# Kernel optimization log

Measured on AMD Instinct MI355X. Metric: run time of the kernel, lower is better.

Reference implementation:

```python
import jax, jax.numpy as jnp
import numpy as np

IMSIZE = 128; R = 2; B = 2; C = 3; D = 64; Q = 128; M = 8; ITERS = 32
N = IMSIZE * IMSIZE
EPS = 1e-8


def _build_edges(S, r):
    # local (2r+1)^2 pixel neighborhood, as in build_perception(imsize, perception_size)
    ys, xs = np.meshgrid(np.arange(S), np.arange(S), indexing='ij')
    rows, cols = [], []
    for dy in range(-r, r + 1):
        for dx in range(-r, r + 1):
            ny, nx = ys + dy, xs + dx
            ok = (ny >= 0) & (ny < S) & (nx >= 0) & (nx < S)
            rows.append((ys * S + xs)[ok])
            cols.append((ny * S + nx)[ok])
    return (np.concatenate(rows).astype(np.int32), np.concatenate(cols).astype(np.int32))


def _conv(x, w, b=None):
    y = jax.lax.conv_general_dilated(x, w, (1, 1), 'SAME', dimension_numbers=('NHWC', 'HWIO', 'NHWC'))
    return y if b is None else y + b


def _bn(x, g, b):
    mu = x.mean((0, 1, 2))
    var = x.var((0, 1, 2))
    return (x - mu) * jax.lax.rsqrt(var + 1e-5) * g + b


def _resblock(f, w1, g1, t1, w2, g2, t2):
    h = jax.nn.relu(_bn(_conv(f, w1), g1, t1))
    h = _bn(_conv(h, w2), g2, t2)
    return jax.nn.relu(f + h)


def _forward(x, w_bb1, b_bb1, w_bb2, b_bb2,
             w_k1, g_k1, t_k1, w_k2, g_k2, t_k2, w_kp, b_kp,
             w_q1, g_q1, t_q1, w_q2, g_q2, t_q2, w_qp,
             h0, row, col, agent_idx):
    # conv backbone (preserves spatial resolution)
    f = jax.nn.relu(_conv(x, w_bb1, b_bb1))
    f = jax.nn.relu(_conv(f, w_bb2, b_bb2))
    # key / query heads: ResidualBlock + 1x1 conv
    ks = _conv(_resblock(f, w_k1, g_k1, t_k1, w_k2, g_k2, t_k2), w_kp, b_kp).reshape(B, N, D)
    qs = _conv(_resblock(f, w_q1, g_q1, t_q1, w_q2, g_q2, t_q2), w_qp).reshape(B, N, D)
    # edge-gather cosine similarity (torch.cosine_similarity with eps=1e-8)
    qe = qs[:, row]          # [B, E, D]
    ke = ks[:, col]          # [B, E, D]
    weights = (qe * ke).sum(-1) / (
        jnp.maximum(jnp.linalg.norm(qe, axis=-1), EPS) *
        jnp.maximum(jnp.linalg.norm(ke, axis=-1), EPS))   # [B, E]

    # 32-iteration sparse adjacency propagation: h <- normalize(A @ h)
    def step(h, _):
        msg = jnp.zeros_like(h).at[:, row, :].add(weights[:, :, None] * h[:, col, :])
        h = msg / jnp.maximum(jnp.linalg.norm(msg, axis=-1, keepdims=True), EPS)
        return h, None

    h, _ = jax.lax.scan(step, h0, None, length=ITERS)     # [B, N, Q]

    # competition routing: pixels compete for M agent slots via cosine affinity
    pix = h / jnp.maximum(jnp.linalg.norm(h, axis=-1, keepdims=True), EPS)
    ag = pix[:, agent_idx]                                # [B, M, Q]
    sim = jnp.einsum('bnq,bmq->bnm', pix, ag)
    masks = jax.nn.softmax(sim * 10.0, axis=-1)           # [B, N, M]
    return masks.reshape(B, IMSIZE, IMSIZE, M).transpose(0, 3, 1, 2)  # [B, M, W, H]


def setup_inputs() -> dict:
    key = jax.random.key(0)
    k = jax.random.split(key, 12)
    s = 0.05
    row, col = _build_edges(IMSIZE, R)
    agent_idx = np.linspace(0, N - 1, M).astype(np.int32)
    return dict(
        x=jax.random.normal(k[0], (B, IMSIZE, IMSIZE, C), jnp.float32),
        w_bb1=jax.random.normal(k[1], (3, 3, C, D), jnp.float32) * s, b_bb1=jnp.zeros((D,), jnp.float32),
        w_bb2=jax.random.normal(k[2], (3, 3, D, D), jnp.float32) * s, b_bb2=jnp.zeros((D,), jnp.float32),
        w_k1=jax.random.normal(k[3], (3, 3, D, D), jnp.float32) * s,
        g_k1=jnp.ones((D,), jnp.float32), t_k1=jnp.zeros((D,), jnp.float32),
        w_k2=jax.random.normal(k[4], (3, 3, D, D), jnp.float32) * s,
        g_k2=jnp.ones((D,), jnp.float32), t_k2=jnp.zeros((D,), jnp.float32),
        w_kp=jax.random.normal(k[5], (1, 1, D, D), jnp.float32) * s, b_kp=jnp.zeros((D,), jnp.float32),
        w_q1=jax.random.normal(k[6], (3, 3, D, D), jnp.float32) * s,
        g_q1=jnp.ones((D,), jnp.float32), t_q1=jnp.zeros((D,), jnp.float32),
        w_q2=jax.random.normal(k[7], (3, 3, D, D), jnp.float32) * s,
        g_q2=jnp.ones((D,), jnp.float32), t_q2=jnp.zeros((D,), jnp.float32),
        w_qp=jax.random.normal(k[8], (1, 1, D, D), jnp.float32) * s,
        h0=jax.random.normal(k[9], (B, N, Q), jnp.float32),
        row=jnp.asarray(row), col=jnp.asarray(col),
        agent_idx=jnp.asarray(agent_idx),
    )


def reference(x, w_bb1, b_bb1, w_bb2, b_bb2,
              w_k1, g_k1, t_k1, w_k2, g_k2, t_k2, w_kp, b_kp,
              w_q1, g_q1, t_q1, w_q2, g_q2, t_q2, w_qp,
              h0, row, col, agent_idx):
    return _forward(x, w_bb1, b_bb1, w_bb2, b_bb2,
                    w_k1, g_k1, t_k1, w_k2, g_k2, t_k2, w_kp, b_kp,
                    w_q1, g_q1, t_q1, w_q2, g_q2, t_q2, w_qp,
                    h0, row, col, agent_idx)
```

## Files before the change

### kernel.cpp

```cpp
#include <hip/hip_runtime.h>
#include <math.h>

#define NPIX 16384
#define EPSF 1e-8f

typedef float f32x4 __attribute__((ext_vector_type(4)));
typedef short s16x8 __attribute__((ext_vector_type(8)));

__device__ __forceinline__ float wred64(float s){
  s += __shfl_xor(s, 32); s += __shfl_xor(s, 16); s += __shfl_xor(s, 8);
  s += __shfl_xor(s, 4);  s += __shfl_xor(s, 2);  s += __shfl_xor(s, 1);
  return s;
}
__device__ __forceinline__ float rdlane(float v, int l){
  return __int_as_float(__builtin_amdgcn_readlane(__float_as_int(v), l));
}
__device__ __forceinline__ float dot4f(float4 a, float4 b, float acc){
  acc = fmaf(a.x,b.x,acc); acc = fmaf(a.y,b.y,acc);
  acc = fmaf(a.z,b.z,acc); acc = fmaf(a.w,b.w,acc);
  return acc;
}
__device__ __forceinline__ void bf16split(float v, unsigned short &hi, unsigned short &lo){
  unsigned u = __float_as_uint(v);
  unsigned r = u + 0x7FFFu + ((u >> 16) & 1u);
  hi = (unsigned short)(r >> 16);
  float hf = __uint_as_float(((unsigned)hi) << 16);
  float l = v - hf;
  unsigned u2 = __float_as_uint(l);
  unsigned r2 = u2 + 0x7FFFu + ((u2 >> 16) & 1u);
  lo = (unsigned short)(r2 >> 16);
}
__device__ __forceinline__ unsigned bf16rne(float x){
  unsigned u = __float_as_uint(x);
  return (u + 0x7FFFu + ((u >> 16) & 1u)) >> 16;
}

__global__ __launch_bounds__(256) void prep_kernel(const float* __restrict__ w_bb2, const float* __restrict__ w_k1,
                            const float* __restrict__ w_k2, const float* __restrict__ w_q1,
                            const float* __restrict__ w_q2, const float* __restrict__ w_kp,
                            const float* __restrict__ w_qp, unsigned short* __restrict__ wh,
                            unsigned short* __restrict__ wl, float* __restrict__ wtp,
                            float* __restrict__ stats){
  int gid = blockIdx.x*256 + threadIdx.x;
  if (gid < 184320){
    int j = gid & 7;
    int t1 = gid >> 3;
    int lane = t1 & 63;
    int t2 = t1 >> 6;
    int kb = t2 % 18;
    int t3 = t2 / 18;
    int ct = t3 & 3;
    int c  = t3 >> 2;
    const float* src = c==0? w_bb2 : c==1? w_k1 : c==2? w_k2 : c==3? w_q1 : w_q2;
    int cout = ct*16 + (lane & 15);
    int k = kb*32 + (lane>>4)*8 + j;
    float v = src[k*64 + cout];
    unsigned short h,l; bf16split(v,h,l);
    wh[gid] = h; wl[gid] = l;
  } else if (gid < 192512){
    int t = gid - 184320; int which = t >> 12; int d = t & 4095;
    const float* src = which ? w_qp : w_kp;
    int k = d & 3, cout = (d>>2) & 63, cin4 = d >> 8;
    wtp[t] = src[(cin4*4 + k)*64 + cout];
  } else if (gid < 193024){
    stats[gid - 192512] = 0.f;
  }
}

__global__ __launch_bounds__(256) void conv1_kernel(const float* __restrict__ x, const float* __restrict__ w,
                                                    const float* __restrict__ bias, float* __restrict__ out){
  int wv = blockIdx.x*4 + (threadIdx.x >> 6);
  int c  = threadIdx.x & 63;
  int p0 = wv << 3;
  int ub = __builtin_amdgcn_readfirstlane(p0);
  int b  = ub >> 14; int i0 = ub & (NPIX-1);
  int y  = i0 >> 7, x0 = i0 & 127;
  float wv_[9][3];
  #pragma unroll
  for (int t=0;t<9;++t)
    #pragma unroll
    for (int ci=0;ci<3;++ci) wv_[t][ci] = w[(t*3+ci)*64 + c];
  float bv = bias[c];
  float acc[8];
  #pragma unroll
  for (int p=0;p<8;++p) acc[p] = bv;
  for (int ky=0; ky<3; ++ky){
    int ny = y + ky - 1;
    if ((unsigned)ny >= 128u) continue;
    const float* rowp = x + ((b<<14) + ny*128)*3;
    for (int kx=0; kx<3; ++kx){
      int t = ky*3 + kx;
      #pragma unroll
      for (int p=0;p<8;++p){
        int col = x0 + p + kx - 1;
        if ((unsigned)col < 128u){
          const float* ip = rowp + col*3;
          acc[p] = fmaf(ip[0], wv_[t][0], acc[p]);
          acc[p] = fmaf(ip[1], wv_[t][1], acc[p]);
          acc[p] = fmaf(ip[2], wv_[t][2], acc[p]);
        }
      }
    }
  }
  float* op = out + (p0 << 6) + c;
  #pragma unroll
  for (int p=0;p<8;++p) op[p*64] = fmaxf(acc[p], 0.f);
}

__global__ __launch_bounds__(512) void conv3m_kernel(const float* __restrict__ in,
    const unsigned short* __restrict__ wh, const unsigned short* __restrict__ wl,
    const float* __restrict__ bias, int relu,
    const float* __restrict__ bnst, const float* __restrict__ bng, const float* __restrict__ bnb,
    float* __restrict__ out, float* __restrict__ ost){
  __shared__ char smem[50688];
  float* lout = (float*)smem;
  __shared__ float la[64], lb[64];
  __shared__ float ls1[64], ls2[64];
  int blk = blockIdx.x;
  int xh = blk & 1, y = (blk>>1) & 127, b = blk >> 8;
  int x0 = xh << 6;
  int tid = threadIdx.x;
  if (tid < 64){
    float a = 1.f, bo = 0.f;
    if (bnst){
      float mu  = bnst[tid] * (1.f/32768.f);
      float var = bnst[64+tid] * (1.f/32768.f) - mu*mu;
      a  = bng[tid] * rsqrtf(var + 1e-5f);
      bo = bnb[tid] - mu*a;
    }
    la[tid] = a; lb[tid] = bo;
    ls1[tid] = 0.f; ls2[tid] = 0.f;
  }
  __syncthreads();
  for (int s = tid; s < 3168; s += 512){
    int pr = s >> 4, cq = s & 15;
    int ky = pr / 66, px = pr - ky*66;
    int ny = y + ky - 1, gx = x0 - 1 + px;
    float v0=0.f, v1=0.f, v2=0.f, v3=0.f;
    if ((unsigned)ny < 128u && (unsigned)gx < 128u){
      const float* ip = in + (((b<<14) + ny*128 + gx)<<6) + (cq<<2);
      float4 t = *(const float4*)ip;
      int c0 = cq<<2;
      v0 = fmaxf(fmaf(t.x, la[c0],   lb[c0]),   0.f);
      v1 = fmaxf(fmaf(t.y, la[c0+1], lb[c0+1]), 0.f);
      v2 = fmaxf(fmaf(t.z, la[c0+2], lb[c0+2]), 0.f);
      v3 = fmaxf(fmaf(t.w, la[c0+3], lb[c0+3]), 0.f);
    }
    unsigned short h0,l0,h1,l1,h2,l2,h3,l3;
    bf16split(v0,h0,l0); bf16split(v1,h1,l1); bf16split(v2,h2,l2); bf16split(v3,h3,l3);
    int slot = (cq >> 1) ^ (pr & 7);
    int byte = pr*128 + (slot<<4) + ((cq & 1) << 3);
    *(uint2*)(smem + byte) = make_uint2((unsigned)h0 | ((unsigned)h1<<16),
                                        (unsigned)h2 | ((unsigned)h3<<16));
    *(uint2*)(smem + 25344 + byte) = make_uint2((unsigned)l0 | ((unsigned)l1<<16),
                                                (unsigned)l2 | ((unsigned)l3<<16));
  }
  __syncthreads();
  int lane = tid & 63, wid = tid >> 6;
  int pxsub = wid & 3, ch = wid >> 2;
  int col16 = lane & 15, kgrp = lane >> 4;
  f32x4 acc0 = {0.f,0.f,0.f,0.f}, acc1 = acc0, acl0 = acc0, acl1 = acc0;
  int abase = (ch*2*18)*512 + lane*8;
  #pragma unroll
  for (int kb=0; kb<18; ++kb){
    int tap = kb >> 1;
    int ky = (tap >= 6) ? 2 : (tap >= 3 ? 1 : 0);
    int kx = tap - ky*3;
    int pr = ky*66 + pxsub*16 + col16 + kx;
    int ci0 = ((kb & 1) << 5) + (kgrp << 3);
    int byte = pr*128 + ((((ci0 >> 3) ^ (pr & 7))) << 4);
    s16x8 Bh = *(const s16x8*)(smem + byte);
    s16x8 Bl = *(const s16x8*)(smem + 25344 + byte);
    int ao = abase + kb*512;
    s16x8 Ah0 = *(const s16x8*)(wh + ao);
    s16x8 Al0 = *(const s16x8*)(wl + ao);
    s16x8 Ah1 = *(const s16x8*)(wh + ao + 9216);
    s16x8 Al1 = *(const s16x8*)(wl + ao + 9216);
    acc0 = __builtin_amdgcn_mfma_f32_16x16x32_bf16(Ah0, Bh, acc0, 0, 0, 0);
    acl0 = __builtin_amdgcn_mfma_f32_16x16x32_bf16(Ah0, Bl, acl0, 0, 0, 0);
    acc1 = __builtin_amdgcn_mfma_f32_16x16x32_bf16(Ah1, Bh, acc1, 0, 0, 0);
    acl1 = __builtin_amdgcn_mfma_f32_16x16x32_bf16(Ah1, Bl, acl1, 0, 0, 0);
    acl0 = __builtin_amdgcn_mfma_f32_16x16x32_bf16(Al0, Bh, acl0, 0, 0, 0);
    acl1 = __builtin_amdgcn_mfma_f32_16x16x32_bf16(Al1, Bh, acl1, 0, 0, 0);
  }
  acc0 = acc0 + acl0;
  acc1 = acc1 + acl1;
  __syncthreads();
  int pxl = pxsub*16 + col16;
  int co0 = ch*32 + kgrp*4;
  *(f32x4*)(lout + pxl*68 + co0)      = acc0;
  *(f32x4*)(lout + pxl*68 + co0 + 16) = acc1;
  __syncthreads();
  {
    int px = tid >> 3, c8 = (tid & 7) << 3;
    const float* lp = lout + px*68 + c8;
    float r0[8];
    #pragma unroll
    for (int j=0;j<8;++j) r0[j] = lp[j];
    if (bias){
      #pragma unroll
      for (int j=0;j<8;++j) r0[j] += bias[c8+j];
    }
    if (relu){
      #pragma unroll
      for (int j=0;j<8;++j) r0[j] = fmaxf(r0[j], 0.f);
    }
    float* op = out + (((b<<14) + y*128 + x0 + px)<<6) + c8;
    #pragma unroll
    for (int j=0;j<8;++j) op[j] = r0[j];
    if (ost){
      float s1v[8], s2v[8];
      #pragma unroll
      for (int j=0;j<8;++j){ s1v[j] = r0[j]; s2v[j] = r0[j]*r0[j]; }
      #pragma unroll
      for (int m=8; m<64; m<<=1){
        #pragma unroll
        for (int j=0;j<8;++j){ s1v[j] += __shfl_xor(s1v[j], m); s2v[j] += __shfl_xor(s2v[j], m); }
      }
      int lane2 = tid & 63;
      if ((lane2 >> 3) == 0){
        int c0 = (lane2 & 7) << 3;
        #pragma unroll
        for (int j=0;j<8;++j){ atomicAdd(&ls1[c0+j], s1v[j]); atomicAdd(&ls2[c0+j], s2v[j]); }
      }
      __syncthreads();
      if (tid < 64){ atomicAdd(&ost[tid], ls1[tid]); atomicAdd(&ost[64+tid], ls2[tid]); }
    }
  }
}

__global__ __launch_bounds__(512) void conv3m2_kernel(const float* __restrict__ in,
    const unsigned short* __restrict__ whA, const unsigned short* __restrict__ wlA,
    const unsigned short* __restrict__ whB, const unsigned short* __restrict__ wlB,
    float* __restrict__ outA, float* __restrict__ ostA,
    float* __restrict__ outB, float* __restrict__ ostB){
  __shared__ char smem[50688];
  float* loutA = (float*)smem;
  float* loutB = (float*)smem + 4352;
  __shared__ float ls1A[64], ls2A[64], ls1B[64], ls2B[64];
  int blk = blockIdx.x;
  int xh = blk & 1, y = (blk>>1) & 127, b = blk >> 8;
  int x0 = xh << 6;
  int tid = threadIdx.x;
  if (tid < 64){ ls1A[tid]=0.f; ls2A[tid]=0.f; ls1B[tid]=0.f; ls2B[tid]=0.f; }
  __syncthreads();
  for (int s = tid; s < 3168; s += 512){
    int pr = s >> 4, cq = s & 15;
    int ky = pr / 66, px = pr - ky*66;
    int ny = y + ky - 1, gx = x0 - 1 + px;
    float v0=0.f, v1=0.f, v2=0.f, v3=0.f;
    if ((unsigned)ny < 128u && (unsigned)gx < 128u){
      const float* ip = in + (((b<<14) + ny*128 + gx)<<6) + (cq<<2);
      float4 t = *(const float4*)ip;
      v0 = t.x; v1 = t.y; v2 = t.z; v3 = t.w;
    }
    unsigned short h0,l0,h1,l1,h2,l2,h3,l3;
    bf16split(v0,h0,l0); bf16split(v1,h1,l1); bf16split(v2,h2,l2); bf16split(v3,h3,l3);
    int slot = (cq >> 1) ^ (pr & 7);
    int byte = pr*128 + (slot<<4) + ((cq & 1) << 3);
    *(uint2*)(smem + byte) = make_uint2((unsigned)h0 | ((unsigned)h1<<16),
                                        (unsigned)h2 | ((unsigned)h3<<16));
    *(uint2*)(smem + 25344 + byte) = make_uint2((unsigned)l0 | ((unsigned)l1<<16),
                                                (unsigned)l2 | ((unsigned)l3<<16));
  }
  __syncthreads();
  int lane = tid & 63, wid = tid >> 6;
  int pxsub = wid & 3, ch = wid >> 2;
  int col16 = lane & 15, kgrp = lane >> 4;
  f32x4 z = {0.f,0.f,0.f,0.f};
  f32x4 aA0=z, aA1=z, lA0=z, lA1=z, aB0=z, aB1=z, lB0=z, lB1=z;
  int abase = (ch*2*18)*512 + lane*8;
  #pragma unroll
  for (int kb=0; kb<18; ++kb){
    int tap = kb >> 1;
    int ky = (tap >= 6) ? 2 : (tap >= 3 ? 1 : 0);
    int kx = tap - ky*3;
    int pr = ky*66 + pxsub*16 + col16 + kx;
    int ci0 = ((kb & 1) << 5) + (kgrp << 3);
    int byte = pr*128 + ((((ci0 >> 3) ^ (pr & 7))) << 4);
    s16x8 Bh = *(const s16x8*)(smem + byte);
    s16x8 Bl = *(const s16x8*)(smem + 25344 + byte);
    int ao = abase + kb*512;
    s16x8 AhA0 = *(const s16x8*)(whA + ao);
    s16x8 AlA0 = *(const s16x8*)(wlA + ao);
    s16x8 AhA1 = *(const s16x8*)(whA + ao + 9216);
    s16x8 AlA1 = *(const s16x8*)(wlA + ao + 9216);
    s16x8 AhB0 = *(const s16x8*)(whB + ao);
    s16x8 AlB0 = *(const s16x8*)(wlB + ao);
    s16x8 AhB1 = *(const s16x8*)(whB + ao + 9216);
    s16x8 AlB1 = *(const s16x8*)(wlB + ao + 9216);
    aA0 = __builtin_amdgcn_mfma_f32_16x16x32_bf16(AhA0, Bh, aA0, 0, 0, 0);
    lA0 = __builtin_amdgcn_mfma_f32_16x16x32_bf16(AhA0, Bl, lA0, 0, 0, 0);
    aA1 = __builtin_amdgcn_mfma_f32_16x16x32_bf16(AhA1, Bh, aA1, 0, 0, 0);
    lA1 = __builtin_amdgcn_mfma_f32_16x16x32_bf16(AhA1, Bl, lA1, 0, 0, 0);
    lA0 = __builtin_amdgcn_mfma_f32_16x16x32_bf16(AlA0, Bh, lA0, 0, 0, 0);
    lA1 = __builtin_amdgcn_mfma_f32_16x16x32_bf16(AlA1, Bh, lA1, 0, 0, 0);
    aB0 = __builtin_amdgcn_mfma_f32_16x16x32_bf16(AhB0, Bh, aB0, 0, 0, 0);
    lB0 = __builtin_amdgcn_mfma_f32_16x16x32_bf16(AhB0, Bl, lB0, 0, 0, 0);
    aB1 = __builtin_amdgcn_mfma_f32_16x16x32_bf16(AhB1, Bh, aB1, 0, 0, 0);
    lB1 = __builtin_amdgcn_mfma_f32_16x16x32_bf16(AhB1, Bl, lB1, 0, 0, 0);
    lB0 = __builtin_amdgcn_mfma_f32_16x16x32_bf16(AlB0, Bh, lB0, 0, 0, 0);
    lB1 = __builtin_amdgcn_mfma_f32_16x16x32_bf16(AlB1, Bh, lB1, 0, 0, 0);
  }
  aA0 = aA0 + lA0; aA1 = aA1 + lA1;
  aB0 = aB0 + lB0; aB1 = aB1 + lB1;
  __syncthreads();
  int pxl = pxsub*16 + col16;
  int co0 = ch*32 + kgrp*4;
  *(f32x4*)(loutA + pxl*68 + co0)      = aA0;
  *(f32x4*)(loutA + pxl*68 + co0 + 16) = aA1;
  *(f32x4*)(loutB + pxl*68 + co0)      = aB0;
  *(f32x4*)(loutB + pxl*68 + co0 + 16) = aB1;
  __syncthreads();
  {
    int px = tid >> 3, c8 = (tid & 7) << 3;
    int lane2 = tid & 63;
    float rA[8], rB[8];
    #pragma unroll
    for (int j=0;j<8;++j){ rA[j] = loutA[px*68 + c8 + j]; rB[j] = loutB[px*68 + c8 + j]; }
    float* opA = outA + (((b<<14) + y*128 + x0 + px)<<6) + c8;
    float* opB = outB + (((b<<14) + y*128 + x0 + px)<<6) + c8;
    #pragma unroll
    for (int j=0;j<8;++j){ opA[j] = rA[j]; opB[j] = rB[j]; }
    float sA1[8], sA2[8], sB1[8], sB2[8];
    #pragma unroll
    for (int j=0;j<8;++j){ sA1[j]=rA[j]; sA2[j]=rA[j]*rA[j]; sB1[j]=rB[j]; sB2[j]=rB[j]*rB[j]; }
    #pragma unroll
    for (int m=8; m<64; m<<=1){
      #pragma unroll
      for (int j=0;j<8;++j){
        sA1[j] += __shfl_xor(sA1[j], m); sA2[j] += __shfl_xor(sA2[j], m);
        sB1[j] += __shfl_xor(sB1[j], m); sB2[j] += __shfl_xor(sB2[j], m);
      }
    }
    if ((lane2 >> 3) == 0){
      int c0 = (lane2 & 7) << 3;
      #pragma unroll
      for (int j=0;j<8;++j){
        atomicAdd(&ls1A[c0+j], sA1[j]); atomicAdd(&ls2A[c0+j], sA2[j]);
        atomicAdd(&ls1B[c0+j], sB1[j]); atomicAdd(&ls2B[c0+j], sB2[j]);
      }
    }
    __syncthreads();
    if (tid < 64){
      atomicAdd(&ostA[tid], ls1A[tid]); atomicAdd(&ostA[64+tid], ls2A[tid]);
      atomicAdd(&ostB[tid], ls1B[tid]); atomicAdd(&ostB[64+tid], ls2B[tid]);
    }
  }
}

__global__ __launch_bounds__(256) void resfuse2_kernel(float* __restrict__ tk, float* __restrict__ tq,
                                                       const float* __restrict__ f, const float* __restrict__ ST,
                                                       const float* __restrict__ gk, const float* __restrict__ bk,
                                                       const float* __restrict__ gq, const float* __restrict__ bq){
  int gid = blockIdx.x*256 + threadIdx.x;
  int isQ = gid >> 19;
  int idx4 = gid & 524287;
  float* t = isQ ? tq : tk;
  const float* stats = ST + (isQ ? 384 : 128);
  const float* g    = isQ ? gq : gk;
  const float* beta = isQ ? bq : bk;
  float4 v = ((float4*)t)[idx4];
  float4 fv = ((const float4*)f)[idx4];
  int c0 = (idx4 & 15) * 4;
  float a[4], bb[4];
  #pragma unroll
  for (int j=0;j<4;++j){
    int c = c0 + j;
    float mu  = stats[c]    * (1.f/32768.f);
    float var = stats[64+c] * (1.f/32768.f) - mu*mu;
    a[j]  = g[c] * rsqrtf(var + 1e-5f);
    bb[j] = beta[c] - mu*a[j];
  }
  v.x = fmaxf(fv.x + fmaf(v.x, a[0], bb[0]), 0.f);
  v.y = fmaxf(fv.y + fmaf(v.y, a[1], bb[1]), 0.f);
  v.z = fmaxf(fv.z + fmaf(v.z, a[2], bb[2]), 0.f);
  v.w = fmaxf(fv.w + fmaf(v.w, a[3], bb[3]), 0.f);
  ((float4*)t)[idx4] = v;
}

__global__ __launch_bounds__(256) void proj2_kernel(const float* __restrict__ rk, const float* __restrict__ rq,
                                                    const float* __restrict__ wtp, const float* __restrict__ bkp,
                                                    float* __restrict__ outk, float* __restrict__ outq,
                                                    float* __restrict__ nk, float* __restrict__ nq){
  int wvg = blockIdx.x*4 + (threadIdx.x >> 6);
  int isQ = wvg >> 12;
  int wv = wvg & 4095;
  int c  = threadIdx.x & 63;
  const float* r = isQ ? rq : rk;
  const float* wt1 = wtp + (isQ ? 4096 : 0);
  float* out = isQ ? outq : outk;
  float* nrm = isQ ? nq : nk;
  int p0 = wv << 3;
  int ub = __builtin_amdgcn_readfirstlane(p0);
  const float4* wq = (const float4*)wt1 + c;
  float4 w[16];
  #pragma unroll
  for (int q=0;q<16;++q) w[q] = wq[q*64];
  float bv = isQ ? 0.f : bkp[c];
  #pragma unroll
  for (int p=0;p<8;++p){
    const float* ip = r + ((ub + p) << 6);
    float a0 = bv, a1 = 0.f;
    #pragma unroll
    for (int q=0;q<16;q+=2){
      float4 i0 = *(const float4*)(ip + (q<<2));
      float4 i1 = *(const float4*)(ip + ((q+1)<<2));
      a0 = dot4f(i0, w[q],   a0);
      a1 = dot4f(i1, w[q+1], a1);
    }
    float acc = a0 + a1;
    out[((p0+p)<<6) + c] = acc;
    float s = wred64(acc*acc);
    if (c == 0) nrm[p0+p] = sqrtf(s);
  }
}

#define EW_PAD 68
__global__ __launch_bounds__(256) void edge_kernel(const float* __restrict__ qs, const float* __restrict__ ks,
                                                   const float* __restrict__ nq, const float* __restrict__ nk,
                                                   float* __restrict__ W){
  __shared__ float klds[100*EW_PAD];
  __shared__ float qlds[16*EW_PAD];
  int blk = blockIdx.x;
  int b = blk >> 10; int rem = blk & 1023;
  int y = rem >> 3; int x0 = (rem & 7) << 4;
  int tid = threadIdx.x;
  for (int s = tid; s < 1600; s += 256){
    int cin4 = s & 15; int col = (s >> 4) % 20; int r = (s >> 4) / 20;
    int ry = y - 2 + r; ry = ry < 0 ? 0 : (ry > 127 ? 127 : ry);
    int cx = x0 - 2 + col; cx = cx < 0 ? 0 : (cx > 127 ? 127 : cx);
    float4 v = *(const float4*)(ks + (((b<<14) + ry*128 + cx)<<6) + cin4*4);
    *(float4*)(klds + (r*20+col)*EW_PAD + cin4*4) = v;
  }
  {
    int cin4 = tid & 15; int px = tid >> 4;
    float4 v = *(const float4*)(qs + (((b<<14) + y*128 + x0 + px)<<6) + cin4*4);
    *(float4*)(qlds + px*EW_PAD + cin4*4) = v;
  }
  __syncthreads();
  #pragma unroll
  for (int pair=0; pair<2; ++pair){
    int t2 = tid + pair*256;
    int px = t2 >> 5; int o = t2 & 31;
    if (o < 25){
      int dy = o/5 - 2, dx = o%5 - 2;
      int yy = y + dy, xx = x0 + px + dx;
      bool valid = ((unsigned)yy < 128u) && ((unsigned)xx < 128u);
      const float* kq = klds + ((dy+2)*20 + (px+dx+2))*EW_PAD;
      const float* qq = qlds + px*EW_PAD;
      float a0 = 0.f, a1 = 0.f;
      #pragma unroll
      for (int q=0; q<16; q+=2){
        a0 = dot4f(*(const float4*)(qq + q*4),     *(const float4*)(kq + q*4),     a0);
        a1 = dot4f(*(const float4*)(qq + (q+1)*4), *(const float4*)(kq + (q+1)*4), a1);
      }
      float acc = a0 + a1;
      int gp = (b<<14) + y*128 + x0 + px;
      float wv_ = 0.f;
      if (valid){
        int gj = (b<<14) + yy*128 + xx;
        float rq = 1.f / fmaxf(nq[gp], EPSF);
        float rk = 1.f / fmaxf(nk[gj], EPSF);
        wv_ = acc * rq * rk;
      }
      W[gp*25 + o] = wv_;
    }
  }
}

__global__ __launch_bounds__(256) void mp_first_kernel(const float* __restrict__ src, unsigned* __restrict__ dst,
                                                       const float* __restrict__ W){
  int lane = threadIdx.x & 63;
  int wid  = threadIdx.x >> 6;
  int blk  = blockIdx.x;
  int xcd = blk & 7, s = blk >> 3;
  int row_id = xcd*32 + (s >> 3);
  int q8 = s & 7;
  int b = row_id >> 7, y = row_id & 127;
  int x0 = ((q8 << 2) + wid) << 2;
  int gp0 = (b << 14) + y*128 + x0;
  int lo = lane < 25 ? lane : 24;
  float wv[4];
  #pragma unroll
  for (int p=0;p<4;++p) wv[p] = W[(gp0+p)*25 + lo];
  const float* rp[5];
  #pragma unroll
  for (int r=0;r<5;++r){
    int ry = y - 2 + r; ry = ry < 0 ? 0 : (ry > 127 ? 127 : ry);
    rp[r] = src + (((b<<14) + ry*128) << 7) + lane;
  }
  float wa[5][5], wb[5][5];
  #pragma unroll
  for (int cc=0; cc<4; ++cc){
    int xc = x0 - 2 + cc; if (xc < 0) xc = 0;
    int off = xc << 7;
    #pragma unroll
    for (int r=0;r<5;++r){ wa[r][cc] = rp[r][off]; wb[r][cc] = rp[r][off + 64]; }
  }
  #pragma unroll
  for (int p=0;p<4;++p){
    int xl = x0 + p + 2; if (xl > 127) xl = 127;
    int off = xl << 7;
    #pragma unroll
    for (int r=0;r<5;++r){ wa[r][4] = rp[r][off]; wb[r][4] = rp[r][off + 64]; }
    float a0 = 0.f, a1 = 0.f;
    #pragma unroll
    for (int r=0;r<5;++r){
      #pragma unroll
      for (int cc=0;cc<5;++cc){
        float w = rdlane(wv[p], r*5+cc);
        a0 = fmaf(w, wa[r][cc], a0);
        a1 = fmaf(w, wb[r][cc], a1);
      }
    }
    float ss = wred64(a0*a0 + a1*a1);
    float sc = 1.f / fmaxf(sqrtf(ss), EPSF);
    dst[((gp0 + p) << 6) + lane] = (bf16rne(a1*sc) << 16) | bf16rne(a0*sc);
    #pragma unroll
    for (int r=0;r<5;++r){
      #pragma unroll
      for (int cc=0;cc<4;++cc){ wa[r][cc] = wa[r][cc+1]; wb[r][cc] = wb[r][cc+1]; }
    }
  }
}

__global__ __launch_bounds__(256) void mp_iterb_kernel(const unsigned* __restrict__ src, unsigned* __restrict__ dst,
                                                       const float* __restrict__ W){
  int lane = threadIdx.x & 63;
  int wid  = threadIdx.x >> 6;
  int blk  = blockIdx.x;
  int xcd = blk & 7, s = blk >> 3;
  int row_id = xcd*32 + (s >> 3);
  int q8 = s & 7;
  int b = row_id >> 7, y = row_id & 127;
  int x0 = ((q8 << 2) + wid) << 2;
  int gp0 = (b << 14) + y*128 + x0;
  int lo = lane < 25 ? lane : 24;
  float wv[4];
  #pragma unroll
  for (int p=0;p<4;++p) wv[p] = W[(gp0+p)*25 + lo];
  const unsigned* rp[5];
  #pragma unroll
  for (int r=0;r<5;++r){
    int ry = y - 2 + r; ry = ry < 0 ? 0 : (ry > 127 ? 127 : ry);
    rp[r] = src + (((b<<14) + ry*128) << 6) + lane;
  }
  float wa[5][5], wb[5][5];
  #pragma unroll
  for (int cc=0; cc<4; ++cc){
    int xc = x0 - 2 + cc; if (xc < 0) xc = 0;
    int off = xc << 6;
    #pragma unroll
    for (int r=0;r<5;++r){
      unsigned v = rp[r][off];
      wa[r][cc] = __uint_as_float(v << 16);
      wb[r][cc] = __uint_as_float(v & 0xffff0000u);
    }
  }
  #pragma unroll
  for (int p=0;p<4;++p){
    int xl = x0 + p + 2; if (xl > 127) xl = 127;
    int off = xl << 6;
    #pragma unroll
    for (int r=0;r<5;++r){
      unsigned v = rp[r][off];
      wa[r][4] = __uint_as_float(v << 16);
      wb[r][4] = __uint_as_float(v & 0xffff0000u);
    }
    float a0 = 0.f, a1 = 0.f;
    #pragma unroll
    for (int r=0;r<5;++r){
      #pragma unroll
      for (int cc=0;cc<5;++cc){
        float w = rdlane(wv[p], r*5+cc);
        a0 = fmaf(w, wa[r][cc], a0);
        a1 = fmaf(w, wb[r][cc], a1);
      }
    }
    float ss = wred64(a0*a0 + a1*a1);
    float sc = 1.f / fmaxf(sqrtf(ss), EPSF);
    dst[((gp0 + p) << 6) + lane] = (bf16rne(a1*sc) << 16) | bf16rne(a0*sc);
    #pragma unroll
    for (int r=0;r<5;++r){
      #pragma unroll
      for (int cc=0;cc<4;++cc){ wa[r][cc] = wa[r][cc+1]; wb[r][cc] = wb[r][cc+1]; }
    }
  }
}

__global__ __launch_bounds__(256) void mp_lastb_kernel(const unsigned* __restrict__ src, const float* __restrict__ W,
                                                       const int* __restrict__ agidx, float* __restrict__ out){
  int lane = threadIdx.x & 63;
  int wid  = threadIdx.x >> 6;
  int blk  = blockIdx.x;
  int xcd = blk & 7, s = blk >> 3;
  int row_id = xcd*32 + (s >> 2);
  int q4 = s & 3;
  int b = row_id >> 7, y = row_id & 127;
  int x0 = ((q4 << 2) + wid) << 3;
  int gp0 = (b << 14) + y*128 + x0;
  int lo = lane < 25 ? lane : 24;
  float av0[8], av1[8], isc[8];
  #pragma unroll
  for (int m=0;m<8;++m){
    int ai = agidx[m];
    int ay = ai >> 7, ax = ai & 127;
    float wva = W[((b<<14) + ai)*25 + lo];
    float aa0 = 0.f, aa1 = 0.f;
    #pragma unroll
    for (int r=0;r<5;++r){
      int ry = ay - 2 + r; ry = ry < 0 ? 0 : (ry > 127 ? 127 : ry);
      const unsigned* rp = src + (((b<<14) + ry*128) << 6) + lane;
      #pragma unroll
      for (int cc=0;cc<5;++cc){
        int xc = ax - 2 + cc; xc = xc < 0 ? 0 : (xc > 127 ? 127 : xc);
        unsigned v = rp[xc<<6];
        float w = rdlane(wva, r*5+cc);
        aa0 = fmaf(w, __uint_as_float(v << 16), aa0);
        aa1 = fmaf(w, __uint_as_float(v & 0xffff0000u), aa1);
      }
    }
    float ssm = wred64(aa0*aa0 + aa1*aa1);
    isc[m] = 1.f / fmaxf(sqrtf(ssm), EPSF);
    av0[m] = aa0; av1[m] = aa1;
  }
  float wv[8];
  #pragma unroll
  for (int p=0;p<8;++p) wv[p] = W[(gp0+p)*25 + lo];
  const unsigned* rp[5];
  #pragma unroll
  for (int r=0;r<5;++r){
    int ry = y - 2 + r; ry = ry < 0 ? 0 : (ry > 127 ? 127 : ry);
    rp[r] = src + (((b<<14) + ry*128) << 6) + lane;
  }
  float wa[5][5], wb[5][5];
  #pragma unroll
  for (int cc=0; cc<4; ++cc){
    int xc = x0 - 2 + cc; if (xc < 0) xc = 0;
    int off = xc << 6;
    #pragma unroll
    for (int r=0;r<5;++r){
      unsigned v = rp[r][off];
      wa[r][cc] = __uint_as_float(v << 16);
      wb[r][cc] = __uint_as_float(v & 0xffff0000u);
    }
  }
  #pragma unroll
  for (int p=0;p<8;++p){
    int xl = x0 + p + 2; if (xl > 127) xl = 127;
    int off = xl << 6;
    #pragma unroll
    for (int r=0;r<5;++r){
      unsigned v = rp[r][off];
      wa[r][4] = __uint_as_float(v << 16);
      wb[r][4] = __uint_as_float(v & 0xffff0000u);
    }
    float a0 = 0.f, a1 = 0.f;
    #pragma unroll
    for (int r=0;r<5;++r){
      #pragma unroll
      for (int cc=0;cc<5;++cc){
        float w = rdlane(wv[p], r*5+cc);
        a0 = fmaf(w, wa[r][cc], a0);
        a1 = fmaf(w, wb[r][cc], a1);
      }
    }
    float ss = wred64(a0*a0 + a1*a1);
    float sc = 1.f / fmaxf(sqrtf(ss), EPSF);
    float p0 = a0*sc, p1 = a1*sc;
    float sim[8];
    #pragma unroll
    for (int m=0;m<8;++m)
      sim[m] = wred64(p0*av0[m] + p1*av1[m]) * isc[m];
    float mx = sim[0];
    #pragma unroll
    for (int m=1;m<8;++m) mx = fmaxf(mx, sim[m]);
    float e[8]; float sum = 0.f;
    #pragma unroll
    for (int m=0;m<8;++m){ e[m] = __expf((sim[m]-mx)*10.f); sum += e[m]; }
    float rs = 1.f / sum;
    if (lane < 8){
      float val = e[0];
      #pragma unroll
      for (int m=1;m<8;++m) val = (lane==m) ? e[m] : val;
      out[(((b<<3)+lane)<<14) + y*128 + x0 + p] = val * rs;
    }
    #pragma unroll
    for (int r=0;r<5;++r){
      #pragma unroll
      for (int cc=0;cc<4;++cc){ wa[r][cc] = wa[r][cc+1]; wb[r][cc] = wb[r][cc+1]; }
    }
  }
}

extern "C" void kernel_launch(void* const* d_in, const int* in_sizes, int n_in,
                              void* d_out, int out_size, void* d_ws, size_t ws_size,
                              hipStream_t stream) {
  (void)in_sizes; (void)n_in; (void)out_size; (void)ws_size;
  const float* x     = (const float*)d_in[0];
  const float* w_bb1 = (const float*)d_in[1];
  const float* b_bb1 = (const float*)d_in[2];
  const float* w_bb2 = (const float*)d_in[3];
  const float* b_bb2 = (const float*)d_in[4];
  const float* w_k1  = (const float*)d_in[5];
  const float* g_k1  = (const float*)d_in[6];
  const float* t_k1  = (const float*)d_in[7];
  const float* w_k2  = (const float*)d_in[8];
  const float* g_k2  = (const float*)d_in[9];
  const float* t_k2  = (const float*)d_in[10];
  const float* w_kp  = (const float*)d_in[11];
  const float* b_kp  = (const float*)d_in[12];
  const float* w_q1  = (const float*)d_in[13];
  const float* g_q1  = (const float*)d_in[14];
  const float* t_q1  = (const float*)d_in[15];
  const float* w_q2  = (const float*)d_in[16];
  const float* g_q2  = (const float*)d_in[17];
  const float* t_q2  = (const float*)d_in[18];
  const float* w_qp  = (const float*)d_in[19];
  const float* h0    = (const float*)d_in[20];
  const int*   agidx = (const int*)d_in[23];
  float* out = (float*)d_out;
  float* ws  = (float*)d_ws;

  float* S0 = ws + 0;
  float* S1 = ws + 2097152;
  float* S2 = ws + 4194304;
  float* S3 = ws + 6291456;
  float* S4 = ws + 8388608;
  float* WW = ws + 12582912;
  float* NK = ws + 13402112;
  float* NQ = ws + 13434880;
  float* ST = ws + 13467648;
  float* WTp = ws + 13470208;
  unsigned short* WH = (unsigned short*)(ws + 13478400);
  unsigned short* WL = WH + 184320;
  unsigned* BA = (unsigned*)(ws + 0);
  unsigned* BB = (unsigned*)(ws + 2097152);

  prep_kernel<<<754, 256, 0, stream>>>(w_bb2, w_k1, w_k2, w_q1, w_q2, w_kp, w_qp, WH, WL, WTp, ST);
  conv1_kernel<<<1024, 256, 0, stream>>>(x, w_bb1, b_bb1, S0);
  conv3m_kernel<<<512, 512, 0, stream>>>(S0, WH + 0, WL + 0, b_bb2, 1, nullptr, nullptr, nullptr, S1, nullptr);
  conv3m2_kernel<<<512, 512, 0, stream>>>(S1, WH + 36864, WL + 36864, WH + 3*36864, WL + 3*36864,
                                          S2, ST + 0, S3, ST + 256);
  conv3m_kernel<<<512, 512, 0, stream>>>(S2, WH + 2*36864, WL + 2*36864, nullptr, 0, ST + 0, g_k1, t_k1, S0, ST + 128);
  conv3m_kernel<<<512, 512, 0, stream>>>(S3, WH + 4*36864, WL + 4*36864, nullptr, 0, ST + 256, g_q1, t_q1, S2, ST + 384);
  resfuse2_kernel<<<4096, 256, 0, stream>>>(S0, S2, S1, ST, g_k2, t_k2, g_q2, t_q2);
  proj2_kernel<<<2048, 256, 0, stream>>>(S0, S2, WTp, b_kp, S4, S3, NK, NQ);
  edge_kernel<<<2048, 256, 0, stream>>>(S3, S4, NQ, NK, WW);
  mp_first_kernel<<<2048, 256, 0, stream>>>(h0, BA, WW);
  const unsigned* sb = BA;
  for (int it = 0; it < 30; ++it){
    unsigned* db = (it & 1) ? BA : BB;
    mp_iterb_kernel<<<2048, 256, 0, stream>>>(sb, db, WW);
    sb = db;
  }
  mp_lastb_kernel<<<1024, 256, 0, stream>>>(sb, WW, agidx, out);
}
```

Before: 581.4 us.

## Merge key/query second convs into one launch and fuse residual-BN into projection

The key and query second-conv launches are combined into a single 1024-block kernel that picks its inputs, weights and BN stats by block half. This doubles the grid of one launch and removes a launch boundary. The separate residual+BN+ReLU elementwise kernel is removed, and that work is folded into the 1x1 projection kernel, which now reads the conv output and the backbone features and applies the BN affine on the fly. This avoids one full read/write pass over two 64-channel activation tensors, at the cost of extra loads and ALU work inside the projection, and buffer assignments are remapped to match.

```diff
diff --git a/kernel.cpp b/kernel.cpp
--- a/kernel.cpp
+++ b/kernel.cpp
@@ -109,29 +109,13 @@
 
 __global__ __launch_bounds__(512) void conv3m_kernel(const float* __restrict__ in,
     const unsigned short* __restrict__ wh, const unsigned short* __restrict__ wl,
-    const float* __restrict__ bias, int relu,
-    const float* __restrict__ bnst, const float* __restrict__ bng, const float* __restrict__ bnb,
-    float* __restrict__ out, float* __restrict__ ost){
+    const float* __restrict__ bias, int relu, float* __restrict__ out){
   __shared__ char smem[50688];
   float* lout = (float*)smem;
-  __shared__ float la[64], lb[64];
-  __shared__ float ls1[64], ls2[64];
   int blk = blockIdx.x;
   int xh = blk & 1, y = (blk>>1) & 127, b = blk >> 8;
   int x0 = xh << 6;
   int tid = threadIdx.x;
-  if (tid < 64){
-    float a = 1.f, bo = 0.f;
-    if (bnst){
-      float mu  = bnst[tid] * (1.f/32768.f);
-      float var = bnst[64+tid] * (1.f/32768.f) - mu*mu;
-      a  = bng[tid] * rsqrtf(var + 1e-5f);
-      bo = bnb[tid] - mu*a;
-    }
-    la[tid] = a; lb[tid] = bo;
-    ls1[tid] = 0.f; ls2[tid] = 0.f;
-  }
-  __syncthreads();
   for (int s = tid; s < 3168; s += 512){
     int pr = s >> 4, cq = s & 15;
     int ky = pr / 66, px = pr - ky*66;
@@ -140,11 +124,7 @@
     if ((unsigned)ny < 128u && (unsigned)gx < 128u){
       const float* ip = in + (((b<<14) + ny*128 + gx)<<6) + (cq<<2);
       float4 t = *(const float4*)ip;
-      int c0 = cq<<2;
-      v0 = fmaxf(fmaf(t.x, la[c0],   lb[c0]),   0.f);
-      v1 = fmaxf(fmaf(t.y, la[c0+1], lb[c0+1]), 0.f);
-      v2 = fmaxf(fmaf(t.z, la[c0+2], lb[c0+2]), 0.f);
-      v3 = fmaxf(fmaf(t.w, la[c0+3], lb[c0+3]), 0.f);
+      v0 = t.x; v1 = t.y; v2 = t.z; v3 = t.w;
     }
     unsigned short h0,l0,h1,l1,h2,l2,h3,l3;
     bf16split(v0,h0,l0); bf16split(v1,h1,l1); bf16split(v2,h2,l2); bf16split(v3,h3,l3);
@@ -208,24 +188,6 @@
     float* op = out + (((b<<14) + y*128 + x0 + px)<<6) + c8;
     #pragma unroll
     for (int j=0;j<8;++j) op[j] = r0[j];
-    if (ost){
-      float s1v[8], s2v[8];
-      #pragma unroll
-      for (int j=0;j<8;++j){ s1v[j] = r0[j]; s2v[j] = r0[j]*r0[j]; }
-      #pragma unroll
-      for (int m=8; m<64; m<<=1){
-        #pragma unroll
-        for (int j=0;j<8;++j){ s1v[j] += __shfl_xor(s1v[j], m); s2v[j] += __shfl_xor(s2v[j], m); }
-      }
-      int lane2 = tid & 63;
-      if ((lane2 >> 3) == 0){
-        int c0 = (lane2 & 7) << 3;
-        #pragma unroll
-        for (int j=0;j<8;++j){ atomicAdd(&ls1[c0+j], s1v[j]); atomicAdd(&ls2[c0+j], s2v[j]); }
-      }
-      __syncthreads();
-      if (tid < 64){ atomicAdd(&ost[tid], ls1[tid]); atomicAdd(&ost[64+tid], ls2[tid]); }
-    }
   }
 }
 
@@ -349,44 +311,149 @@
   }
 }
 
-__global__ __launch_bounds__(256) void resfuse2_kernel(float* __restrict__ tk, float* __restrict__ tq,
-                                                       const float* __restrict__ f, const float* __restrict__ ST,
-                                                       const float* __restrict__ gk, const float* __restrict__ bk,
-                                                       const float* __restrict__ gq, const float* __restrict__ bq){
-  int gid = blockIdx.x*256 + threadIdx.x;
-  int isQ = gid >> 19;
-  int idx4 = gid & 524287;
-  float* t = isQ ? tq : tk;
-  const float* stats = ST + (isQ ? 384 : 128);
-  const float* g    = isQ ? gq : gk;
-  const float* beta = isQ ? bq : bk;
-  float4 v = ((float4*)t)[idx4];
-  float4 fv = ((const float4*)f)[idx4];
-  int c0 = (idx4 & 15) * 4;
-  float a[4], bb[4];
-  #pragma unroll
-  for (int j=0;j<4;++j){
-    int c = c0 + j;
-    float mu  = stats[c]    * (1.f/32768.f);
-    float var = stats[64+c] * (1.f/32768.f) - mu*mu;
-    a[j]  = g[c] * rsqrtf(var + 1e-5f);
-    bb[j] = beta[c] - mu*a[j];
-  }
-  v.x = fmaxf(fv.x + fmaf(v.x, a[0], bb[0]), 0.f);
-  v.y = fmaxf(fv.y + fmaf(v.y, a[1], bb[1]), 0.f);
-  v.z = fmaxf(fv.z + fmaf(v.z, a[2], bb[2]), 0.f);
-  v.w = fmaxf(fv.w + fmaf(v.w, a[3], bb[3]), 0.f);
-  ((float4*)t)[idx4] = v;
-}
-
-__global__ __launch_bounds__(256) void proj2_kernel(const float* __restrict__ rk, const float* __restrict__ rq,
-                                                    const float* __restrict__ wtp, const float* __restrict__ bkp,
-                                                    float* __restrict__ outk, float* __restrict__ outq,
-                                                    float* __restrict__ nk, float* __restrict__ nq){
-  int wvg = blockIdx.x*4 + (threadIdx.x >> 6);
+__global__ __launch_bounds__(512) void conv3mD_kernel(const float* __restrict__ inK, const float* __restrict__ inQ,
+    const unsigned short* __restrict__ whK, const unsigned short* __restrict__ wlK,
+    const unsigned short* __restrict__ whQ, const unsigned short* __restrict__ wlQ,
+    float* __restrict__ ST, const float* __restrict__ gk, const float* __restrict__ tk,
+    const float* __restrict__ gq, const float* __restrict__ tq,
+    float* __restrict__ outK, float* __restrict__ outQ){
+  __shared__ char smem[50688];
+  float* lout = (float*)smem;
+  __shared__ float la[64], lb[64];
+  __shared__ float ls1[64], ls2[64];
+  int blk = blockIdx.x;
+  int half = blk >> 9;
+  int inner = blk & 511;
+  int xh = inner & 1, y = (inner>>1) & 127, b = inner >> 8;
+  int x0 = xh << 6;
+  const float* in = half ? inQ : inK;
+  const unsigned short* wh = half ? whQ : whK;
+  const unsigned short* wl = half ? wlQ : wlK;
+  const float* bnst = ST + (half ? 256 : 0);
+  const float* bng  = half ? gq : gk;
+  const float* bnb  = half ? tq : tk;
+  float* out = half ? outQ : outK;
+  float* ost = ST + (half ? 384 : 128);
+  int tid = threadIdx.x;
+  if (tid < 64){
+    float mu  = bnst[tid] * (1.f/32768.f);
+    float var = bnst[64+tid] * (1.f/32768.f) - mu*mu;
+    float a = bng[tid] * rsqrtf(var + 1e-5f);
+    la[tid] = a; lb[tid] = bnb[tid] - mu*a;
+    ls1[tid] = 0.f; ls2[tid] = 0.f;
+  }
+  __syncthreads();
+  for (int s = tid; s < 3168; s += 512){
+    int pr = s >> 4, cq = s & 15;
+    int ky = pr / 66, px = pr - ky*66;
+    int ny = y + ky - 1, gx = x0 - 1 + px;
+    float v0=0.f, v1=0.f, v2=0.f, v3=0.f;
+    if ((unsigned)ny < 128u && (unsigned)gx < 128u){
+      const float* ip = in + (((b<<14) + ny*128 + gx)<<6) + (cq<<2);
+      float4 t = *(const float4*)ip;
+      int c0 = cq<<2;
+      v0 = fmaxf(fmaf(t.x, la[c0],   lb[c0]),   0.f);
+      v1 = fmaxf(fmaf(t.y, la[c0+1], lb[c0+1]), 0.f);
+      v2 = fmaxf(fmaf(t.z, la[c0+2], lb[c0+2]), 0.f);
+      v3 = fmaxf(fmaf(t.w, la[c0+3], lb[c0+3]), 0.f);
+    }
+    unsigned short h0,l0,h1,l1,h2,l2,h3,l3;
+    bf16split(v0,h0,l0); bf16split(v1,h1,l1); bf16split(v2,h2,l2); bf16split(v3,h3,l3);
+    int slot = (cq >> 1) ^ (pr & 7);
+    int byte = pr*128 + (slot<<4) + ((cq & 1) << 3);
+    *(uint2*)(smem + byte) = make_uint2((unsigned)h0 | ((unsigned)h1<<16),
+                                        (unsigned)h2 | ((unsigned)h3<<16));
+    *(uint2*)(smem + 25344 + byte) = make_uint2((unsigned)l0 | ((unsigned)l1<<16),
+                                                (unsigned)l2 | ((unsigned)l3<<16));
+  }
+  __syncthreads();
+  int lane = tid & 63, wid = tid >> 6;
+  int pxsub = wid & 3, ch = wid >> 2;
+  int col16 = lane & 15, kgrp = lane >> 4;
+  f32x4 acc0 = {0.f,0.f,0.f,0.f}, acc1 = acc0, acl0 = acc0, acl1 = acc0;
+  int abase = (ch*2*18)*512 + lane*8;
+  #pragma unroll
+  for (int kb=0; kb<18; ++kb){
+    int tap = kb >> 1;
+    int ky = (tap >= 6) ? 2 : (tap >= 3 ? 1 : 0);
+    int kx = tap - ky*3;
+    int pr = ky*66 + pxsub*16 + col16 + kx;
+    int ci0 = ((kb & 1) << 5) + (kgrp << 3);
+    int byte = pr*128 + ((((ci0 >> 3) ^ (pr & 7))) << 4);
+    s16x8 Bh = *(const s16x8*)(smem + byte);
+    s16x8 Bl = *(const s16x8*)(smem + 25344 + byte);
+    int ao = abase + kb*512;
+    s16x8 Ah0 = *(const s16x8*)(wh + ao);
+    s16x8 Al0 = *(const s16x8*)(wl + ao);
+    s16x8 Ah1 = *(const s16x8*)(wh + ao + 9216);
+    s16x8 Al1 = *(const s16x8*)(wl + ao + 9216);
+    acc0 = __builtin_amdgcn_mfma_f32_16x16x32_bf16(Ah0, Bh, acc0, 0, 0, 0);
+    acl0 = __builtin_amdgcn_mfma_f32_16x16x32_bf16(Ah0, Bl, acl0, 0, 0, 0);
+    acc1 = __builtin_amdgcn_mfma_f32_16x16x32_bf16(Ah1, Bh, acc1, 0, 0, 0);
+    acl1 = __builtin_amdgcn_mfma_f32_16x16x32_bf16(Ah1, Bl, acl1, 0, 0, 0);
+    acl0 = __builtin_amdgcn_mfma_f32_16x16x32_bf16(Al0, Bh, acl0, 0, 0, 0);
+    acl1 = __builtin_amdgcn_mfma_f32_16x16x32_bf16(Al1, Bh, acl1, 0, 0, 0);
+  }
+  acc0 = acc0 + acl0;
+  acc1 = acc1 + acl1;
+  __syncthreads();
+  int pxl = pxsub*16 + col16;
+  int co0 = ch*32 + kgrp*4;
+  *(f32x4*)(lout + pxl*68 + co0)      = acc0;
+  *(f32x4*)(lout + pxl*68 + co0 + 16) = acc1;
+  __syncthreads();
+  {
+    int px = tid >> 3, c8 = (tid & 7) << 3;
+    const float* lp = lout + px*68 + c8;
+    float r0[8];
+    #pragma unroll
+    for (int j=0;j<8;++j) r0[j] = lp[j];
+    float* op = out + (((b<<14) + y*128 + x0 + px)<<6) + c8;
+    #pragma unroll
+    for (int j=0;j<8;++j) op[j] = r0[j];
+    float s1v[8], s2v[8];
+    #pragma unroll
+    for (int j=0;j<8;++j){ s1v[j] = r0[j]; s2v[j] = r0[j]*r0[j]; }
+    #pragma unroll
+    for (int m=8; m<64; m<<=1){
+      #pragma unroll
+      for (int j=0;j<8;++j){ s1v[j] += __shfl_xor(s1v[j], m); s2v[j] += __shfl_xor(s2v[j], m); }
+    }
+    int lane2 = tid & 63;
+    if ((lane2 >> 3) == 0){
+      int c0 = (lane2 & 7) << 3;
+      #pragma unroll
+      for (int j=0;j<8;++j){ atomicAdd(&ls1[c0+j], s1v[j]); atomicAdd(&ls2[c0+j], s2v[j]); }
+    }
+    __syncthreads();
+    if (tid < 64){ atomicAdd(&ost[tid], ls1[tid]); atomicAdd(&ost[64+tid], ls2[tid]); }
+  }
+}
+
+__global__ __launch_bounds__(256) void proj2f_kernel(const float* __restrict__ rk, const float* __restrict__ rq,
+    const float* __restrict__ f, const float* __restrict__ ST,
+    const float* __restrict__ gk, const float* __restrict__ bk2,
+    const float* __restrict__ gq, const float* __restrict__ bq2,
+    const float* __restrict__ wtp, const float* __restrict__ bkp,
+    float* __restrict__ outk, float* __restrict__ outq,
+    float* __restrict__ nk, float* __restrict__ nq){
+  __shared__ __align__(16) float la[64];
+  __shared__ __align__(16) float lb[64];
+  int tid = threadIdx.x;
+  int wvg = blockIdx.x*4 + (tid >> 6);
   int isQ = wvg >> 12;
+  if (tid < 64){
+    const float* stats = ST + (isQ ? 384 : 128);
+    const float* g    = isQ ? gq : gk;
+    const float* beta = isQ ? bq2 : bk2;
+    float mu  = stats[tid] * (1.f/32768.f);
+    float var = stats[64+tid] * (1.f/32768.f) - mu*mu;
+    float a = g[tid] * rsqrtf(var + 1e-5f);
+    la[tid] = a; lb[tid] = beta[tid] - mu*a;
+  }
+  __syncthreads();
   int wv = wvg & 4095;
-  int c  = threadIdx.x & 63;
+  int c  = tid & 63;
   const float* r = isQ ? rq : rk;
   const float* wt1 = wtp + (isQ ? 4096 : 0);
   float* out = isQ ? outq : outk;
@@ -401,13 +468,30 @@
   #pragma unroll
   for (int p=0;p<8;++p){
     const float* ip = r + ((ub + p) << 6);
+    const float* fp = f + ((ub + p) << 6);
     float a0 = bv, a1 = 0.f;
     #pragma unroll
     for (int q=0;q<16;q+=2){
-      float4 i0 = *(const float4*)(ip + (q<<2));
-      float4 i1 = *(const float4*)(ip + ((q+1)<<2));
-      a0 = dot4f(i0, w[q],   a0);
-      a1 = dot4f(i1, w[q+1], a1);
+      float4 t0 = *(const float4*)(ip + (q<<2));
+      float4 f0 = *(const float4*)(fp + (q<<2));
+      float4 A0 = *(const float4*)(la + (q<<2));
+      float4 B0 = *(const float4*)(lb + (q<<2));
+      float4 r0;
+      r0.x = fmaxf(f0.x + fmaf(t0.x, A0.x, B0.x), 0.f);
+      r0.y = fmaxf(f0.y + fmaf(t0.y, A0.y, B0.y), 0.f);
+      r0.z = fmaxf(f0.z + fmaf(t0.z, A0.z, B0.z), 0.f);
+      r0.w = fmaxf(f0.w + fmaf(t0.w, A0.w, B0.w), 0.f);
+      a0 = dot4f(r0, w[q], a0);
+      float4 t1 = *(const float4*)(ip + ((q+1)<<2));
+      float4 f1 = *(const float4*)(fp + ((q+1)<<2));
+      float4 A1 = *(const float4*)(la + ((q+1)<<2));
+      float4 B1 = *(const float4*)(lb + ((q+1)<<2));
+      float4 r1;
+      r1.x = fmaxf(f1.x + fmaf(t1.x, A1.x, B1.x), 0.f);
+      r1.y = fmaxf(f1.y + fmaf(t1.y, A1.y, B1.y), 0.f);
+      r1.z = fmaxf(f1.z + fmaf(t1.z, A1.z, B1.z), 0.f);
+      r1.w = fmaxf(f1.w + fmaf(t1.w, A1.w, B1.w), 0.f);
+      a1 = dot4f(r1, w[q+1], a1);
     }
     float acc = a0 + a1;
     out[((p0+p)<<6) + c] = acc;
@@ -740,14 +824,14 @@
 
   prep_kernel<<<754, 256, 0, stream>>>(w_bb2, w_k1, w_k2, w_q1, w_q2, w_kp, w_qp, WH, WL, WTp, ST);
   conv1_kernel<<<1024, 256, 0, stream>>>(x, w_bb1, b_bb1, S0);
-  conv3m_kernel<<<512, 512, 0, stream>>>(S0, WH + 0, WL + 0, b_bb2, 1, nullptr, nullptr, nullptr, S1, nullptr);
+  conv3m_kernel<<<512, 512, 0, stream>>>(S0, WH + 0, WL + 0, b_bb2, 1, S1);
   conv3m2_kernel<<<512, 512, 0, stream>>>(S1, WH + 36864, WL + 36864, WH + 3*36864, WL + 3*36864,
                                           S2, ST + 0, S3, ST + 256);
-  conv3m_kernel<<<512, 512, 0, stream>>>(S2, WH + 2*36864, WL + 2*36864, nullptr, 0, ST + 0, g_k1, t_k1, S0, ST + 128);
-  conv3m_kernel<<<512, 512, 0, stream>>>(S3, WH + 4*36864, WL + 4*36864, nullptr, 0, ST + 256, g_q1, t_q1, S2, ST + 384);
-  resfuse2_kernel<<<4096, 256, 0, stream>>>(S0, S2, S1, ST, g_k2, t_k2, g_q2, t_q2);
-  proj2_kernel<<<2048, 256, 0, stream>>>(S0, S2, WTp, b_kp, S4, S3, NK, NQ);
-  edge_kernel<<<2048, 256, 0, stream>>>(S3, S4, NQ, NK, WW);
+  conv3mD_kernel<<<1024, 512, 0, stream>>>(S2, S3, WH + 2*36864, WL + 2*36864, WH + 4*36864, WL + 4*36864,
+                                           ST, g_k1, t_k1, g_q1, t_q1, S0, S4);
+  proj2f_kernel<<<2048, 256, 0, stream>>>(S0, S4, S1, ST, g_k2, t_k2, g_q2, t_q2,
+                                          WTp, b_kp, S2, S3, NK, NQ);
+  edge_kernel<<<2048, 256, 0, stream>>>(S3, S2, NQ, NK, WW);
   mp_first_kernel<<<2048, 256, 0, stream>>>(h0, BA, WW);
   const unsigned* sb = BA;
   for (int it = 0; it < 30; ++it){
```

Measured after the change: 570.9 us. About the same (-1.8%).
